# Performance work log

Measured on AMD Instinct MI355X. Metric: run time of the kernel, lower is better.

Reference implementation:

```python
import jax, jax.numpy as jnp
import numpy as np

EXTENT = 0.5       # init kwarg 'extent'
RES = 256          # init kwarg 'resolution'
BATCH = 8
N_PTS = 65536      # one 256x256 Fourier slice per image


def setup_inputs() -> dict:
    key = jax.random.key(0)
    k1, k2 = jax.random.split(key)
    # coordinates in [-extent, extent]
    x = (jax.random.uniform(k1, (BATCH, N_PTS, 3), dtype=jnp.float32) * 2.0 - 1.0) * EXTENT
    # learned volume parameter, matches 1e-5 * randn init
    volume = 1e-5 * jax.random.normal(k2, (RES, RES, RES), dtype=jnp.float32)
    return {"x": x, "volume": volume}


def _grid_sample_3d(vol, coords):
    """Trilinear grid sample, align_corners=False, padding_mode='zeros'.
    vol: [D, H, W]; coords: [..., 3] with (x, y, z) in [-1, 1] indexing (W, H, D).
    Matches torch.nn.functional.grid_sample(mode='bilinear') for 5D input.
    """
    D, H, W = vol.shape
    gx, gy, gz = coords[..., 0], coords[..., 1], coords[..., 2]
    # unnormalize (align_corners=False): ix = ((x + 1) * W - 1) / 2
    ix = ((gx + 1.0) * W - 1.0) * 0.5
    iy = ((gy + 1.0) * H - 1.0) * 0.5
    iz = ((gz + 1.0) * D - 1.0) * 0.5
    x0 = jnp.floor(ix)
    y0 = jnp.floor(iy)
    z0 = jnp.floor(iz)
    tx = ix - x0  # fractional weights
    ty = iy - y0
    tz = iz - z0
    x0i = x0.astype(jnp.int32)
    y0i = y0.astype(jnp.int32)
    z0i = z0.astype(jnp.int32)

    def corner(dz, dy, dx):
        xi = x0i + dx
        yi = y0i + dy
        zi = z0i + dz
        valid = (xi >= 0) & (xi < W) & (yi >= 0) & (yi < H) & (zi >= 0) & (zi < D)
        v = vol[jnp.clip(zi, 0, D - 1), jnp.clip(yi, 0, H - 1), jnp.clip(xi, 0, W - 1)]
        return jnp.where(valid, v, jnp.zeros((), vol.dtype))

    wx0, wy0, wz0 = 1.0 - tx, 1.0 - ty, 1.0 - tz
    out = (corner(0, 0, 0) * wz0 * wy0 * wx0
           + corner(0, 0, 1) * wz0 * wy0 * tx
           + corner(0, 1, 0) * wz0 * ty * wx0
           + corner(0, 1, 1) * wz0 * ty * tx
           + corner(1, 0, 0) * tz * wy0 * wx0
           + corner(1, 0, 1) * tz * wy0 * tx
           + corner(1, 1, 0) * tz * ty * wx0
           + corner(1, 1, 1) * tz * ty * tx)
    return out


def reference(x, volume):
    # original: grid_sample(100 * volume.repeat(B,...), x/(2*extent)*2)
    #    the linear interpolation (mathematically identical).
    coords = x / EXTENT  # [B, n_pts, 3] in [-1, 1]
    return 100.0 * _grid_sample_3d(volume, coords)  # [B, n_pts]
```

## Files before the change

### kernel.cpp

```cpp
#include <hip/hip_runtime.h>


#define RES 256
#define NB 256
#define CAP 2560
#define WIN 256
#define WINDOWS 10

typedef float vfloat4 __attribute__((ext_vector_type(4)));


__device__ __forceinline__ void setup_c(
    float rx, float ry, float rz,
    int& r00, int& r01, int& r10, int& r11, int& xc0, int& xc1,
    float& wx0, float& wx1, float& wy0, float& wy1, float& wz0, float& wz1)
{
    float gx = rx * 2.0f;
    float gy = ry * 2.0f;
    float gz = rz * 2.0f;

    float ix = ((gx + 1.0f) * (float)RES - 1.0f) * 0.5f;
    float iy = ((gy + 1.0f) * (float)RES - 1.0f) * 0.5f;
    float iz = ((gz + 1.0f) * (float)RES - 1.0f) * 0.5f;

    float x0f = floorf(ix), y0f = floorf(iy), z0f = floorf(iz);
    float tx = ix - x0f, ty = iy - y0f, tz = iz - z0f;

    int x0 = (int)x0f, y0 = (int)y0f, z0 = (int)z0f;
    int x1 = x0 + 1, y1 = y0 + 1, z1 = z0 + 1;

    wx0 = (x0 >= 0 && x0 < RES) ? (1.0f - tx) : 0.0f;
    wx1 = (x1 >= 0 && x1 < RES) ? tx : 0.0f;
    wy0 = (y0 >= 0 && y0 < RES) ? (1.0f - ty) : 0.0f;
    wy1 = (y1 >= 0 && y1 < RES) ? ty : 0.0f;
    wz0 = (z0 >= 0 && z0 < RES) ? (1.0f - tz) : 0.0f;
    wz1 = (z1 >= 0 && z1 < RES) ? tz : 0.0f;

    xc0 = min(max(x0, 0), RES - 1); xc1 = min(max(x1, 0), RES - 1);
    int yc0 = min(max(y0, 0), RES - 1), yc1 = min(max(y1, 0), RES - 1);
    int zc0 = min(max(z0, 0), RES - 1), zc1 = min(max(z1, 0), RES - 1);

    r00 = (zc0 * RES + yc0) * RES;
    r01 = (zc0 * RES + yc1) * RES;
    r10 = (zc1 * RES + yc0) * RES;
    r11 = (zc1 * RES + yc1) * RES;
}

__device__ __forceinline__ void point_setup(
    const float* __restrict__ x, int i,
    int& r00, int& r01, int& r10, int& r11, int& xc0, int& xc1,
    float& wx0, float& wx1, float& wy0, float& wy1, float& wz0, float& wz1)
{
    float rx = __builtin_nontemporal_load(&x[3 * i + 0]);
    float ry = __builtin_nontemporal_load(&x[3 * i + 1]);
    float rz = __builtin_nontemporal_load(&x[3 * i + 2]);
    setup_c(rx, ry, rz, r00, r01, r10, r11, xc0, xc1,
            wx0, wx1, wy0, wy1, wz0, wz1);
}

__device__ __forceinline__ float trilerp(
    const float* __restrict__ vol,
    int r00, int r01, int r10, int r11, int xc0, int xc1,
    float wx0, float wx1, float wy0, float wy1, float wz0, float wz1)
{
    float v000 = vol[r00 + xc0];
    float v001 = vol[r00 + xc1];
    float v010 = vol[r01 + xc0];
    float v011 = vol[r01 + xc1];
    float v100 = vol[r10 + xc0];
    float v101 = vol[r10 + xc1];
    float v110 = vol[r11 + xc0];
    float v111 = vol[r11 + xc1];

    float c00 = v000 * wx0 + v001 * wx1;
    float c01 = v010 * wx0 + v011 * wx1;
    float c10 = v100 * wx0 + v101 * wx1;
    float c11 = v110 * wx0 + v111 * wx1;
    float c0 = c00 * wy0 + c01 * wy1;
    float c1 = c10 * wy0 + c11 * wy1;
    return 100.0f * (c0 * wz0 + c1 * wz1);
}

__device__ __forceinline__ float interp_point(
    const float* __restrict__ vol, float rx, float ry, float rz)
{
    int r00, r01, r10, r11, x0, x1;
    float wx0, wx1, wy0, wy1, wz0, wz1;
    setup_c(rx, ry, rz, r00, r01, r10, r11, x0, x1,
            wx0, wx1, wy0, wy1, wz0, wz1);
    return trilerp(vol, r00, r01, r10, r11, x0, x1,
                   wx0, wx1, wy0, wy1, wz0, wz1);
}


__global__ __launch_bounds__(256) void VolumeExplicit_scatter_kernel(
    const float* __restrict__ x,
    const float* __restrict__ vol,
    float* __restrict__ out,
    vfloat4* __restrict__ sorted,
    unsigned* __restrict__ cursor)
{
    __shared__ unsigned lh[NB];
    __shared__ unsigned lbase[NB];
    int t = threadIdx.x;
    int base_i = blockIdx.x * 1024;

    lh[t] = 0;
    __syncthreads();

    float px[4], py[4], pz[4];
    int bk[4];
    unsigned lr[4];
    #pragma unroll
    for (int k = 0; k < 4; ++k) {
        int i = base_i + (k << 8) + t;
        px[k] = __builtin_nontemporal_load(&x[3 * i + 0]);
        py[k] = __builtin_nontemporal_load(&x[3 * i + 1]);
        pz[k] = __builtin_nontemporal_load(&x[3 * i + 2]);
        float iz = ((pz[k] * 2.0f + 1.0f) * (float)RES - 1.0f) * 0.5f;
        int b = (int)(iz + 0.5f);
        b = min(max(b, 0), NB - 1);
        bk[k] = b;
        lr[k] = atomicAdd(&lh[b], 1u);
    }
    __syncthreads();

    unsigned c = lh[t];
    lbase[t] = c ? atomicAdd(&cursor[t], c) : 0u;
    __syncthreads();

    #pragma unroll
    for (int k = 0; k < 4; ++k) {
        int i = base_i + (k << 8) + t;
        unsigned pos = lbase[bk[k]] + lr[k];
        if (pos < CAP) {
            vfloat4 v;
            v.x = px[k]; v.y = py[k]; v.z = pz[k];
            v.w = __uint_as_float((unsigned)i);
            sorted[bk[k] * CAP + pos] = v;
        } else {
            out[i] = interp_point(vol, px[k], py[k], pz[k]);
        }
    }
}


__global__ __launch_bounds__(256) void VolumeExplicit_gather_kernel(
    const vfloat4* __restrict__ sorted,
    const unsigned* __restrict__ cursor,
    const float* __restrict__ vol,
    float* __restrict__ out)
{
    int t = threadIdx.x;
    int B = blockIdx.x;
    int xcd = B & 7;
    int r = B >> 3;
    int j = r & 15;
    int w = r >> 4;

    #pragma unroll 1
    for (int h = 0; h < 2; ++h) {
        int bucket = xcd * 32 + h * 16 + j;
        unsigned count = min(cursor[bucket], (unsigned)CAP);
        int s = w * WIN + t;
        if ((unsigned)s >= count) continue;

        vfloat4 p = __builtin_nontemporal_load(&sorted[bucket * CAP + s]);

        int r00, r01, r10, r11, x0, x1;
        float wx0, wx1, wy0, wy1, wz0, wz1;
        setup_c(p.x, p.y, p.z, r00, r01, r10, r11, x0, x1,
                wx0, wx1, wy0, wy1, wz0, wz1);
        float o = trilerp(vol, r00, r01, r10, r11, x0, x1,
                          wx0, wx1, wy0, wy1, wz0, wz1);

        __builtin_nontemporal_store(o, &out[__float_as_uint(p.w)]);
    }
}


__global__ __launch_bounds__(256) void VolumeExplicit_29257317220866_kernel(
    const float* __restrict__ x,
    const float* __restrict__ vol,
    float* __restrict__ out,
    int n)
{
    int tid = blockIdx.x * blockDim.x + threadIdx.x;
    int half = n >> 1;
    if (tid >= half) return;
    int iA = tid;
    int iB = tid + half;

    int a_r00, a_r01, a_r10, a_r11, a_x0, a_x1;
    float a_wx0, a_wx1, a_wy0, a_wy1, a_wz0, a_wz1;
    point_setup(x, iA, a_r00, a_r01, a_r10, a_r11, a_x0, a_x1,
                a_wx0, a_wx1, a_wy0, a_wy1, a_wz0, a_wz1);

    int b_r00, b_r01, b_r10, b_r11, b_x0, b_x1;
    float b_wx0, b_wx1, b_wy0, b_wy1, b_wz0, b_wz1;
    point_setup(x, iB, b_r00, b_r01, b_r10, b_r11, b_x0, b_x1,
                b_wx0, b_wx1, b_wy0, b_wy1, b_wz0, b_wz1);

    float oA = trilerp(vol, a_r00, a_r01, a_r10, a_r11, a_x0, a_x1,
                       a_wx0, a_wx1, a_wy0, a_wy1, a_wz0, a_wz1);
    float oB = trilerp(vol, b_r00, b_r01, b_r10, b_r11, b_x0, b_x1,
                       b_wx0, b_wx1, b_wy0, b_wy1, b_wz0, b_wz1);

    __builtin_nontemporal_store(oA, &out[iA]);
    __builtin_nontemporal_store(oB, &out[iB]);
}

extern "C" void kernel_launch(void* const* d_in, const int* in_sizes, int n_in,
                              void* d_out, int out_size, void* d_ws, size_t ws_size,
                              hipStream_t stream) {
    const float* x   = (const float*)d_in[0];
    const float* vol = (const float*)d_in[1];
    float* out = (float*)d_out;

    int n = out_size;
    size_t need = 4096 + (size_t)NB * CAP * sizeof(vfloat4);

    if (n == 524288 && d_ws != nullptr && ws_size >= need) {
        unsigned* cursor = (unsigned*)d_ws;
        vfloat4* sorted  = (vfloat4*)((char*)d_ws + 4096);

        hipMemsetAsync(cursor, 0, NB * sizeof(unsigned), stream);
        VolumeExplicit_scatter_kernel<<<n / 1024, 256, 0, stream>>>(
            x, vol, out, sorted, cursor);
        VolumeExplicit_gather_kernel<<<8 * 16 * WINDOWS, 256, 0, stream>>>(
            sorted, cursor, vol, out);
    } else {
        int half = n >> 1;
        int block = 256;
        int grid = (half + block - 1) / block;
        VolumeExplicit_29257317220866_kernel<<<grid, block, 0, stream>>>(x, vol, out, n);
    }
}
```

Baseline: 133.2 us.

## Bin points into z-y tiles and stage volume slabs in LDS for gathering

Points are now bucketed by their floor z/y cell into 2048 tiles of 4x8 rows instead of 256 z-slices. Each gather block loads the 5x9 rows of volume its tile needs (about 45 KB) into shared memory, then does all eight trilinear lookups from LDS instead of global memory. This replaces scattered global reads with one coalesced slab load per block, but every block pays that load even when its bucket holds few points, and the larger shared-memory footprint limits occupancy. Buckets that overflow the 318-entry cap fall back to direct global interpolation in the scatter kernel.

New measurement: 138.2 us. 3.8% more time.

```diff
diff --git a/kernel.cpp b/kernel.cpp
--- a/kernel.cpp
+++ b/kernel.cpp
@@ -2,10 +2,14 @@
 
 
 #define RES 256
-#define NB 256
-#define CAP 2560
-#define WIN 256
-#define WINDOWS 10
+#define TZ 4
+#define TY 8
+#define NZT 64
+#define NYT 32
+#define NBKT 2048
+#define CAP 318
+#define NROW 45
+#define LDSF (NROW * 256)
 
 typedef float vfloat4 __attribute__((ext_vector_type(4)));
 
@@ -15,13 +19,9 @@
     int& r00, int& r01, int& r10, int& r11, int& xc0, int& xc1,
     float& wx0, float& wx1, float& wy0, float& wy1, float& wz0, float& wz1)
 {
-    float gx = rx * 2.0f;
-    float gy = ry * 2.0f;
-    float gz = rz * 2.0f;
-
-    float ix = ((gx + 1.0f) * (float)RES - 1.0f) * 0.5f;
-    float iy = ((gy + 1.0f) * (float)RES - 1.0f) * 0.5f;
-    float iz = ((gz + 1.0f) * (float)RES - 1.0f) * 0.5f;
+    float ix = ((rx * 2.0f + 1.0f) * (float)RES - 1.0f) * 0.5f;
+    float iy = ((ry * 2.0f + 1.0f) * (float)RES - 1.0f) * 0.5f;
+    float iz = ((rz * 2.0f + 1.0f) * (float)RES - 1.0f) * 0.5f;
 
     float x0f = floorf(ix), y0f = floorf(iy), z0f = floorf(iz);
     float tx = ix - x0f, ty = iy - y0f, tz = iz - z0f;
@@ -46,19 +46,7 @@
     r11 = (zc1 * RES + yc1) * RES;
 }
 
-__device__ __forceinline__ void point_setup(
-    const float* __restrict__ x, int i,
-    int& r00, int& r01, int& r10, int& r11, int& xc0, int& xc1,
-    float& wx0, float& wx1, float& wy0, float& wy1, float& wz0, float& wz1)
-{
-    float rx = __builtin_nontemporal_load(&x[3 * i + 0]);
-    float ry = __builtin_nontemporal_load(&x[3 * i + 1]);
-    float rz = __builtin_nontemporal_load(&x[3 * i + 2]);
-    setup_c(rx, ry, rz, r00, r01, r10, r11, xc0, xc1,
-            wx0, wx1, wy0, wy1, wz0, wz1);
-}
-
-__device__ __forceinline__ float trilerp(
+__device__ __forceinline__ float trilerp_g(
     const float* __restrict__ vol,
     int r00, int r01, int r10, int r11, int xc0, int xc1,
     float wx0, float wx1, float wy0, float wy1, float wz0, float wz1)
@@ -71,7 +59,6 @@
     float v101 = vol[r10 + xc1];
     float v110 = vol[r11 + xc0];
     float v111 = vol[r11 + xc1];
-
     float c00 = v000 * wx0 + v001 * wx1;
     float c01 = v010 * wx0 + v011 * wx1;
     float c10 = v100 * wx0 + v101 * wx1;
@@ -88,8 +75,8 @@
     float wx0, wx1, wy0, wy1, wz0, wz1;
     setup_c(rx, ry, rz, r00, r01, r10, r11, x0, x1,
             wx0, wx1, wy0, wy1, wz0, wz1);
-    return trilerp(vol, r00, r01, r10, r11, x0, x1,
-                   wx0, wx1, wy0, wy1, wz0, wz1);
+    return trilerp_g(vol, r00, r01, r10, r11, x0, x1,
+                     wx0, wx1, wy0, wy1, wz0, wz1);
 }
 
 
@@ -100,12 +87,12 @@
     vfloat4* __restrict__ sorted,
     unsigned* __restrict__ cursor)
 {
-    __shared__ unsigned lh[NB];
-    __shared__ unsigned lbase[NB];
+    __shared__ unsigned lh[NBKT];
+    __shared__ unsigned lbase[NBKT];
     int t = threadIdx.x;
     int base_i = blockIdx.x * 1024;
 
-    lh[t] = 0;
+    for (int b = t; b < NBKT; b += 256) lh[b] = 0;
     __syncthreads();
 
     float px[4], py[4], pz[4];
@@ -117,16 +104,22 @@
         px[k] = __builtin_nontemporal_load(&x[3 * i + 0]);
         py[k] = __builtin_nontemporal_load(&x[3 * i + 1]);
         pz[k] = __builtin_nontemporal_load(&x[3 * i + 2]);
+        float iy = ((py[k] * 2.0f + 1.0f) * (float)RES - 1.0f) * 0.5f;
         float iz = ((pz[k] * 2.0f + 1.0f) * (float)RES - 1.0f) * 0.5f;
-        int b = (int)(iz + 0.5f);
-        b = min(max(b, 0), NB - 1);
-        bk[k] = b;
-        lr[k] = atomicAdd(&lh[b], 1u);
-    }
-    __syncthreads();
-
-    unsigned c = lh[t];
-    lbase[t] = c ? atomicAdd(&cursor[t], c) : 0u;
+        int y0 = (int)floorf(iy);
+        int z0 = (int)floorf(iz);
+        int yc0 = min(max(y0, 0), RES - 1);
+        int zc0 = min(max(z0, 0), RES - 1);
+        int b_ = (zc0 >> 2) * NYT + (yc0 >> 3);
+        bk[k] = b_;
+        lr[k] = atomicAdd(&lh[b_], 1u);
+    }
+    __syncthreads();
+
+    for (int b = t; b < NBKT; b += 256) {
+        unsigned c = lh[b];
+        lbase[b] = c ? atomicAdd(&cursor[b], c) : 0u;
+    }
     __syncthreads();
 
     #pragma unroll
@@ -151,28 +144,80 @@
     const float* __restrict__ vol,
     float* __restrict__ out)
 {
+    __shared__ float smem[LDSF];
+
     int t = threadIdx.x;
     int B = blockIdx.x;
     int xcd = B & 7;
-    int r = B >> 3;
-    int j = r & 15;
-    int w = r >> 4;
-
-    #pragma unroll 1
-    for (int h = 0; h < 2; ++h) {
-        int bucket = xcd * 32 + h * 16 + j;
-        unsigned count = min(cursor[bucket], (unsigned)CAP);
-        int s = w * WIN + t;
-        if ((unsigned)s >= count) continue;
-
+    int j = (B >> 3) & 7;
+    int yt = B >> 6;
+    int zt = xcd * 8 + j;
+    int bucket = zt * NYT + yt;
+
+    for (int k = t; k < NROW * 64; k += 256) {
+        int q = k >> 6;
+        int lane = k & 63;
+        int zr = q / 9;
+        int yr = q - zr * 9;
+        int gz = min(zt * TZ + zr, RES - 1);
+        int gy = min(yt * TY + yr, RES - 1);
+        const vfloat4* src =
+            reinterpret_cast<const vfloat4*>(vol + ((gz << 8) + gy) * 256);
+        reinterpret_cast<vfloat4*>(smem)[(q << 6) + lane] = src[lane];
+    }
+    __syncthreads();
+
+    unsigned count = cursor[bucket];
+    if (count > CAP) count = CAP;
+
+    for (int s = t; s < (int)count; s += 256) {
         vfloat4 p = __builtin_nontemporal_load(&sorted[bucket * CAP + s]);
 
-        int r00, r01, r10, r11, x0, x1;
-        float wx0, wx1, wy0, wy1, wz0, wz1;
-        setup_c(p.x, p.y, p.z, r00, r01, r10, r11, x0, x1,
-                wx0, wx1, wy0, wy1, wz0, wz1);
-        float o = trilerp(vol, r00, r01, r10, r11, x0, x1,
-                          wx0, wx1, wy0, wy1, wz0, wz1);
+        float ix = ((p.x * 2.0f + 1.0f) * (float)RES - 1.0f) * 0.5f;
+        float iy = ((p.y * 2.0f + 1.0f) * (float)RES - 1.0f) * 0.5f;
+        float iz = ((p.z * 2.0f + 1.0f) * (float)RES - 1.0f) * 0.5f;
+
+        float x0f = floorf(ix), y0f = floorf(iy), z0f = floorf(iz);
+        float tx = ix - x0f, ty = iy - y0f, tz = iz - z0f;
+
+        int x0 = (int)x0f, y0 = (int)y0f, z0 = (int)z0f;
+        int x1 = x0 + 1, y1 = y0 + 1, z1 = z0 + 1;
+
+        float wx0 = (x0 >= 0 && x0 < RES) ? (1.0f - tx) : 0.0f;
+        float wx1 = (x1 >= 0 && x1 < RES) ? tx : 0.0f;
+        float wy0 = (y0 >= 0 && y0 < RES) ? (1.0f - ty) : 0.0f;
+        float wy1 = (y1 >= 0 && y1 < RES) ? ty : 0.0f;
+        float wz0 = (z0 >= 0 && z0 < RES) ? (1.0f - tz) : 0.0f;
+        float wz1 = (z1 >= 0 && z1 < RES) ? tz : 0.0f;
+
+        int xc0 = min(max(x0, 0), RES - 1), xc1 = min(max(x1, 0), RES - 1);
+        int yc0 = min(max(y0, 0), RES - 1), yc1 = min(max(y1, 0), RES - 1);
+        int zc0 = min(max(z0, 0), RES - 1), zc1 = min(max(z1, 0), RES - 1);
+
+        int zl0 = zc0 - zt * TZ, zl1 = zc1 - zt * TZ;
+        int yl0 = yc0 - yt * TY, yl1 = yc1 - yt * TY;
+
+        int r00 = ((zl0 * 9 + yl0) << 8);
+        int r01 = ((zl0 * 9 + yl1) << 8);
+        int r10 = ((zl1 * 9 + yl0) << 8);
+        int r11 = ((zl1 * 9 + yl1) << 8);
+
+        float v000 = smem[r00 + xc0];
+        float v001 = smem[r00 + xc1];
+        float v010 = smem[r01 + xc0];
+        float v011 = smem[r01 + xc1];
+        float v100 = smem[r10 + xc0];
+        float v101 = smem[r10 + xc1];
+        float v110 = smem[r11 + xc0];
+        float v111 = smem[r11 + xc1];
+
+        float c00 = v000 * wx0 + v001 * wx1;
+        float c01 = v010 * wx0 + v011 * wx1;
+        float c10 = v100 * wx0 + v101 * wx1;
+        float c11 = v110 * wx0 + v111 * wx1;
+        float c0 = c00 * wy0 + c01 * wy1;
+        float c1 = c10 * wy0 + c11 * wy1;
+        float o = 100.0f * (c0 * wz0 + c1 * wz1);
 
         __builtin_nontemporal_store(o, &out[__float_as_uint(p.w)]);
     }
@@ -191,20 +236,19 @@
     int iA = tid;
     int iB = tid + half;
 
-    int a_r00, a_r01, a_r10, a_r11, a_x0, a_x1;
-    float a_wx0, a_wx1, a_wy0, a_wy1, a_wz0, a_wz1;
-    point_setup(x, iA, a_r00, a_r01, a_r10, a_r11, a_x0, a_x1,
-                a_wx0, a_wx1, a_wy0, a_wy1, a_wz0, a_wz1);
-
-    int b_r00, b_r01, b_r10, b_r11, b_x0, b_x1;
-    float b_wx0, b_wx1, b_wy0, b_wy1, b_wz0, b_wz1;
-    point_setup(x, iB, b_r00, b_r01, b_r10, b_r11, b_x0, b_x1,
-                b_wx0, b_wx1, b_wy0, b_wy1, b_wz0, b_wz1);
-
-    float oA = trilerp(vol, a_r00, a_r01, a_r10, a_r11, a_x0, a_x1,
-                       a_wx0, a_wx1, a_wy0, a_wy1, a_wz0, a_wz1);
-    float oB = trilerp(vol, b_r00, b_r01, b_r10, b_r11, b_x0, b_x1,
-                       b_wx0, b_wx1, b_wy0, b_wy1, b_wz0, b_wz1);
+    float oA, oB;
+    {
+        float rx = __builtin_nontemporal_load(&x[3 * iA + 0]);
+        float ry = __builtin_nontemporal_load(&x[3 * iA + 1]);
+        float rz = __builtin_nontemporal_load(&x[3 * iA + 2]);
+        oA = interp_point(vol, rx, ry, rz);
+    }
+    {
+        float rx = __builtin_nontemporal_load(&x[3 * iB + 0]);
+        float ry = __builtin_nontemporal_load(&x[3 * iB + 1]);
+        float rz = __builtin_nontemporal_load(&x[3 * iB + 2]);
+        oB = interp_point(vol, rx, ry, rz);
+    }
 
     __builtin_nontemporal_store(oA, &out[iA]);
     __builtin_nontemporal_store(oB, &out[iB]);
@@ -218,16 +262,16 @@
     float* out = (float*)d_out;
 
     int n = out_size;
-    size_t need = 4096 + (size_t)NB * CAP * sizeof(vfloat4);
+    size_t need = 8192 + (size_t)NBKT * CAP * sizeof(vfloat4);
 
     if (n == 524288 && d_ws != nullptr && ws_size >= need) {
         unsigned* cursor = (unsigned*)d_ws;
-        vfloat4* sorted  = (vfloat4*)((char*)d_ws + 4096);
-
-        hipMemsetAsync(cursor, 0, NB * sizeof(unsigned), stream);
+        vfloat4* sorted  = (vfloat4*)((char*)d_ws + 8192);
+
+        hipMemsetAsync(cursor, 0, NBKT * sizeof(unsigned), stream);
         VolumeExplicit_scatter_kernel<<<n / 1024, 256, 0, stream>>>(
             x, vol, out, sorted, cursor);
-        VolumeExplicit_gather_kernel<<<8 * 16 * WINDOWS, 256, 0, stream>>>(
+        VolumeExplicit_gather_kernel<<<NBKT, 256, 0, stream>>>(
             sorted, cursor, vol, out);
     } else {
         int half = n >> 1;
```
